# Kernel tuning notes

Hardware: AMD Instinct MI355X
Metric: run time of the kernel (lower is better)

## Reference

```python
import jax, jax.numpy as jnp
import numpy as np

B, N, K = 4, 100000, 128
Q_MIN = 0.5
S_B = 1.0
POT_SCALE = 1.0
REP_SCALE = 1.0
BETA_SCALE = 1.0
E_WEIGHT = 1.0
POS_WEIGHT = 1.0
TIME_WEIGHT = 1.0
HUBER_D = 2.0


def setup_inputs() -> dict:
    key = jax.random.key(0)
    ks = jax.random.split(key, 9)
    return {
        "beta": jax.random.uniform(ks[0], (B, N), dtype=jnp.float32),
        "ccoords": jax.random.normal(ks[1], (B, N, 2), dtype=jnp.float32),
        "pred_energy": jax.random.uniform(ks[2], (B, N), dtype=jnp.float32),
        "pred_pos": jax.random.normal(ks[3], (B, N, 2), dtype=jnp.float32),
        "pred_time": jax.random.uniform(ks[4], (B, N), dtype=jnp.float32),
        "t_energy": jax.random.uniform(ks[5], (B, N), dtype=jnp.float32),
        "t_pos": jax.random.normal(ks[6], (B, N, 2), dtype=jnp.float32),
        "t_time": jax.random.uniform(ks[7], (B, N), dtype=jnp.float32),
        "t_idx": jax.random.randint(ks[8], (B, N), 0, K + 1, dtype=jnp.int32),
    }


def _huber(x, d):
    a = jnp.abs(x)
    return jnp.where(a <= d, 0.5 * x * x, d * (a - 0.5 * d))


def _oc_loss(beta, ccoords, pred_energy, pred_pos, pred_time,
             t_energy, t_pos, t_time, t_idx):
    eps = 1e-4
    beta = jnp.clip(beta, eps, 1.0 - eps)
    q = jnp.arctanh(beta) ** 2 + Q_MIN                     # [B,N]

    obj = t_idx - 1                                        # -1 = noise, 0..K-1 = object id
    M = obj[:, :, None] == jnp.arange(K, dtype=jnp.int32)  # [B,N,K] bool membership
    Mf = M.astype(q.dtype)
    obj_exists = jnp.any(M, axis=1)                        # [B,K]
    exf = obj_exists.astype(q.dtype)

    # condensation point per object = member hit with max charge q (segment argmax)
    q_masked = jnp.where(M, q[:, :, None], -1.0)           # [B,N,K]
    alpha = jnp.argmax(q_masked, axis=1)                   # [B,K]
    x_alpha = jnp.take_along_axis(ccoords, alpha[:, :, None], axis=1)  # [B,K,2]
    q_alpha = jnp.take_along_axis(q, alpha, axis=1)        # [B,K]
    beta_alpha = jnp.take_along_axis(beta, alpha, axis=1)  # [B,K]

    # pairwise hit <-> condensation-point distances, [B,N,K]
    diff = ccoords[:, :, None, :] - x_alpha[:, None, :, :]
    dist = jnp.sqrt(jnp.sum(diff * diff, axis=-1) + 1e-12)

    qq = q[:, :, None] * q_alpha[:, None, :] * exf[:, None, :]
    v_att = qq * (dist * dist) * Mf
    v_rep = qq * jax.nn.relu(1.0 - dist) * (1.0 - Mf)
    n_tot = jnp.asarray(B * N, q.dtype)
    L_att = jnp.sum(v_att) / n_tot
    L_rep = jnp.sum(v_rep) / n_tot

    # beta loss: pull condensation-point betas to 1, suppress noise betas
    n_obj = jnp.maximum(jnp.sum(exf), 1.0)
    L_beta_obj = jnp.sum((1.0 - beta_alpha) * exf) / n_obj
    noise = (t_idx == 0).astype(q.dtype)
    L_noise = jnp.sum(beta * noise) / jnp.maximum(jnp.sum(noise), 1.0)
    L_beta = L_beta_obj + S_B * L_noise

    # payload losses, beta-weighted over non-noise hits
    p = (jnp.arctanh(beta) ** 2) * (1.0 - noise)           # [B,N]
    p_sum = jnp.maximum(jnp.sum(p), 1e-6)
    L_energy = jnp.sum(p * _huber(pred_energy - t_energy, HUBER_D)) / p_sum
    L_pos = jnp.sum(p * jnp.sum((pred_pos - t_pos) ** 2, axis=-1)) / p_sum
    L_time = jnp.sum(p * (pred_time - t_time) ** 2) / p_sum

    return (POT_SCALE * L_att + REP_SCALE * L_rep + BETA_SCALE * L_beta
            + E_WEIGHT * L_energy + POS_WEIGHT * L_pos + TIME_WEIGHT * L_time)


def reference(beta, ccoords, pred_energy, pred_pos, pred_time,
              t_energy, t_pos, t_time, t_idx):
    return _oc_loss(beta, ccoords, pred_energy, pred_pos, pred_time,
                    t_energy, t_pos, t_time, t_idx)
```

## Files before the change

kernel.cpp:

```cpp
#include <hip/hip_runtime.h>
#include <math.h>

#define BB 4
#define NN 100000
#define KK 128
#define HB 512
#define HH 4
#define GX 49
#define NBLK (GX * BB)
#define PB 64


typedef float v2f __attribute__((ext_vector_type(2)));

#if __has_builtin(__builtin_elementwise_fma)
#define FMA2(a, b, c) __builtin_elementwise_fma((a), (b), (c))
#else
static __device__ __forceinline__ v2f fma2_(v2f a, v2f b, v2f c) {
    v2f r; r.x = __builtin_fmaf(a.x, b.x, c.x); r.y = __builtin_fmaf(a.y, b.y, c.y);
    return r;
}
#define FMA2 fma2_
#endif

#if __has_builtin(__builtin_elementwise_max)
#define MAX2(a, b) __builtin_elementwise_max((a), (b))
#else
static __device__ __forceinline__ v2f max2_(v2f a, v2f b) {
    v2f r; r.x = fmaxf(a.x, b.x); r.y = fmaxf(a.y, b.y);
    return r;
}
#define MAX2 max2_
#endif

__device__ __forceinline__ float clipb(float b) {
    return fminf(fmaxf(b, 1e-4f), 1.0f - 1e-4f);
}

__device__ __forceinline__ unsigned long long mkkey(float bf, unsigned n) {
    unsigned hi = __float_as_uint(clipb(bf));
    return ((unsigned long long)hi << 32) |
           (unsigned long long)(0xFFFFFFFFu - n);
}

__global__ void __launch_bounds__(256) k_argmax(
    const float4* __restrict__ beta4, const int4* __restrict__ tidx4,
    unsigned long long* __restrict__ pk_part, unsigned int* __restrict__ cnt) {
    int b = blockIdx.y;
    __shared__ unsigned long long smax[KK];
    for (int t = threadIdx.x; t < KK; t += 256) smax[t] = 0ULL;
    if (blockIdx.x == 0 && b == 0 && threadIdx.x == 0) *cnt = 0u;
    __syncthreads();
    const float4* b4 = beta4 + (size_t)b * (NN / 4);
    const int4*   t4 = tidx4 + (size_t)b * (NN / 4);
    for (int i = blockIdx.x * 256 + threadIdx.x; i < NN / 4; i += PB * 256) {
        float4 bv = b4[i];
        int4   tv = t4[i];
        unsigned n0 = 4u * (unsigned)i;
        if (tv.x > 0) atomicMax(&smax[tv.x - 1], mkkey(bv.x, n0));
        if (tv.y > 0) atomicMax(&smax[tv.y - 1], mkkey(bv.y, n0 + 1));
        if (tv.z > 0) atomicMax(&smax[tv.z - 1], mkkey(bv.z, n0 + 2));
        if (tv.w > 0) atomicMax(&smax[tv.w - 1], mkkey(bv.w, n0 + 3));
    }
    __syncthreads();
    if (threadIdx.x < KK)
        pk_part[((size_t)b * PB + blockIdx.x) * KK + threadIdx.x] =
            smax[threadIdx.x];
}

__global__ void __launch_bounds__(HB) k_main(
    const float*  __restrict__ beta, const float2* __restrict__ cc,
    const float*  __restrict__ pe,   const float2* __restrict__ pp,
    const float*  __restrict__ pt,   const float*  __restrict__ te,
    const float2* __restrict__ tp,   const float*  __restrict__ tt,
    const int*    __restrict__ tidx,
    const unsigned long long* __restrict__ pk_part,
    unsigned long long* __restrict__ final_packed,
    float* __restrict__ part, unsigned int* __restrict__ cnt,
    float* __restrict__ out) {
    int b = blockIdx.y;
    __shared__ v2f sox[KK / 2];
    __shared__ v2f soy[KK / 2];
    __shared__ v2f soq[KK / 2];
    __shared__ float sred[8][8];
    __shared__ unsigned s_last;
    float* sax = (float*)sox;
    float* say = (float*)soy;
    float* saq = (float*)soq;

    if (threadIdx.x < KK) {
        const unsigned long long* src =
            pk_part + ((size_t)b * PB) * KK + threadIdx.x;
        unsigned long long v = 0ULL;
        #pragma unroll 8
        for (int pb = 0; pb < PB; ++pb) {
            unsigned long long u = src[(size_t)pb * KK];
            v = (u > v) ? u : v;
        }
        if (blockIdx.x == 0) final_packed[b * KK + threadIdx.x] = v;
        float x = 0.f, y = 0.f, qz = 0.f;
        if (v) {
            unsigned n = 0xFFFFFFFFu - (unsigned)(v & 0xFFFFFFFFu);
            float ba = __uint_as_float((unsigned)(v >> 32));
            float at = atanhf(ba);
            float2 c = cc[b * NN + (int)n];
            x = c.x; y = c.y; qz = at * at + 0.5f;
        }
        sax[threadIdx.x] = x;
        say[threadIdx.x] = y;
        saq[threadIdx.x] = qz;
    }

    int base = blockIdx.x * (HB * HH) + threadIdx.x;
    bool vv[HH]; int ii[HH]; float rp[HH];
    v2f cx2[HH], cy2[HH];
    #pragma unroll
    for (int h = 0; h < HH; ++h) {
        int n = base + h * HB;
        vv[h] = n < NN;
        ii[h] = b * NN + (vv[h] ? n : 0);
        float2 c = cc[ii[h]];
        cx2[h].x = c.x; cx2[h].y = c.x;
        cy2[h].x = c.y; cy2[h].y = c.y;
        rp[h] = 0.f;
    }
    __syncthreads();

    const v2f eps2 = {1e-12f, 1e-12f};
    const v2f one2 = {1.0f, 1.0f};
    const v2f zero2 = {0.0f, 0.0f};

    #pragma unroll 2
    for (int k2 = 0; k2 < KK / 2; ++k2) {
        v2f ox = sox[k2], oy = soy[k2], oq = soq[k2];
        #pragma unroll
        for (int h = 0; h < HH; ++h) {
            v2f dx = cx2[h] - ox;
            v2f dy = cy2[h] - oy;
            v2f s  = FMA2(dx, dx, FMA2(dy, dy, eps2));
            v2f d;
            d.x = __builtin_amdgcn_sqrtf(s.x);
            d.y = __builtin_amdgcn_sqrtf(s.y);
            v2f r = MAX2(one2 - d, zero2);
            rp[h] = fmaf(oq.x, r.x, rp[h]);
            rp[h] = fmaf(oq.y, r.y, rp[h]);
        }
    }

    float p_att = 0.f, p_rep = 0.f, p_nb = 0.f, p_nc = 0.f;
    float p_ps = 0.f, p_e = 0.f, p_pos = 0.f, p_tm = 0.f;

    #pragma unroll
    for (int h = 0; h < HH; ++h) {
        if (!vv[h]) continue;
        int   idx = ii[h];
        float rep = rp[h];
        float bc  = clipb(beta[idx]);
        float at  = atanhf(bc);
        float at2 = at * at;
        float q   = at2 + 0.5f;
        int   ti  = tidx[idx];
        int   obj = ti - 1;

        if (obj >= 0) {
            float ox = sax[obj], oy = say[obj], oqz = saq[obj];
            float dx = cx2[h].x - ox, dy = cy2[h].x - oy;
            float s = fmaf(dx, dx, fmaf(dy, dy, 1e-12f));
            float d = __builtin_amdgcn_sqrtf(s);
            rep   -= oqz * fmaxf(1.0f - d, 0.0f);
            p_att += q * (oqz * s);
        }
        p_rep += q * rep;

        if (ti == 0) {
            p_nb += bc;
            p_nc += 1.0f;
        } else {
            p_ps += at2;
            float de = pe[idx] - te[idx];
            float a  = fabsf(de);
            float hb = (a <= 2.0f) ? (0.5f * de * de) : (2.0f * (a - 1.0f));
            p_e  += at2 * hb;
            float2 ppv = pp[idx], tpv = tp[idx];
            float dpx = ppv.x - tpv.x, dpy = ppv.y - tpv.y;
            p_pos += at2 * (dpx * dpx + dpy * dpy);
            float dt = pt[idx] - tt[idx];
            p_tm += at2 * dt * dt;
        }
    }

    float vals[8] = {p_att, p_rep, p_nb, p_nc, p_ps, p_e, p_pos, p_tm};
    int lane = threadIdx.x & 63, wave = threadIdx.x >> 6;
    #pragma unroll
    for (int i = 0; i < 8; ++i) {
        float v = vals[i];
        #pragma unroll
        for (int off = 32; off > 0; off >>= 1) v += __shfl_down(v, off, 64);
        if (lane == 0) sred[wave][i] = v;
    }
    __syncthreads();
    if (threadIdx.x < 8) {
        float s = 0.f;
        #pragma unroll
        for (int w = 0; w < HB / 64; ++w) s += sred[w][threadIdx.x];
        part[(b * GX + blockIdx.x) * 8 + threadIdx.x] = s;
    }
    __syncthreads();

    if (threadIdx.x == 0) {
        __threadfence();
        unsigned prev = atomicAdd(cnt, 1u);
        s_last = (prev == (unsigned)(NBLK - 1)) ? 1u : 0u;
    }
    __syncthreads();
    if (s_last) {
        __threadfence();
        if (threadIdx.x < 64) {
            int flane = threadIdx.x;

            float nobj = 0.f, sba = 0.f;
            for (int t = flane; t < BB * KK; t += 64) {
                unsigned long long v = final_packed[t];
                if (v) {
                    nobj += 1.f;
                    sba  += 1.0f - __uint_as_float((unsigned)(v >> 32));
                }
            }
            #pragma unroll
            for (int off = 32; off > 0; off >>= 1) {
                nobj += __shfl_xor(nobj, off, 64);
                sba  += __shfl_xor(sba, off, 64);
            }

            int comp = flane & 7;
            float v = 0.f;
            for (int r = flane >> 3; r < NBLK; r += 8)
                v += part[r * 8 + comp];
            v += __shfl_xor(v, 8, 64);
            v += __shfl_xor(v, 16, 64);
            v += __shfl_xor(v, 32, 64);
            float tot[8];
            #pragma unroll
            for (int c = 0; c < 8; ++c) tot[c] = __shfl(v, c, 64);

            if (flane == 0) {
                float inv_n  = 1.0f / (float)(BB * NN);
                float L_beta = sba / fmaxf(nobj, 1.0f) +
                               tot[2] / fmaxf(tot[3], 1.0f);
                float p_sum  = fmaxf(tot[4], 1e-6f);
                out[0] = tot[0] * inv_n + tot[1] * inv_n + L_beta +
                         (tot[5] + tot[6] + tot[7]) / p_sum;
            }
        }
    }
}

extern "C" void kernel_launch(void* const* d_in, const int* in_sizes, int n_in,
                              void* d_out, int out_size, void* d_ws, size_t ws_size,
                              hipStream_t stream) {
    const float*  beta = (const float*)d_in[0];
    const float2* cc   = (const float2*)d_in[1];
    const float*  pe   = (const float*)d_in[2];
    const float2* pp   = (const float2*)d_in[3];
    const float*  pt   = (const float*)d_in[4];
    const float*  te   = (const float*)d_in[5];
    const float2* tp   = (const float2*)d_in[6];
    const float*  tt   = (const float*)d_in[7];
    const int*    ti   = (const int*)d_in[8];

    unsigned long long* pk_part      = (unsigned long long*)d_ws;
    unsigned long long* final_packed = (unsigned long long*)((char*)d_ws + 262144);
    float*              part         = (float*)((char*)d_ws + 266240);
    unsigned int*       cnt          = (unsigned int*)((char*)d_ws + 272512);
    float*              out          = (float*)d_out;

    k_argmax<<<dim3(PB, BB), 256, 0, stream>>>(
        (const float4*)beta, (const int4*)ti, pk_part, cnt);
    k_main<<<dim3(GX, BB), HB, 0, stream>>>(
        beta, cc, pe, pp, pt, te, tp, tt, ti,
        pk_part, final_packed, part, cnt, out);
}
```

Baseline: 115.1 us.

## Fuse argmax and main pass into one cooperative kernel with grid sync

Merges the segment-argmax kernel into the main kernel. Each block now computes per-object maxima over its own hits, writes per-block partials, and meets the other blocks at a grid-wide barrier before reducing them. Beta, t_idx and coordinates are read once and kept in registers for both phases, and the payload inputs are prefetched before the distance loop. This removes one kernel launch and a second pass over beta/t_idx, at the cost of a cooperative-launch grid sync and higher register pressure.

```diff
diff --git a/kernel.cpp b/kernel.cpp
--- a/kernel.cpp
+++ b/kernel.cpp
@@ -1,5 +1,8 @@
 #include <hip/hip_runtime.h>
+#include <hip/hip_cooperative_groups.h>
 #include <math.h>
+
+namespace cg = cooperative_groups;
 
 #define BB 4
 #define NN 100000
@@ -8,7 +11,6 @@
 #define HH 4
 #define GX 49
 #define NBLK (GX * BB)
-#define PB 64
 
 
 typedef float v2f __attribute__((ext_vector_type(2)));
@@ -43,42 +45,18 @@
            (unsigned long long)(0xFFFFFFFFu - n);
 }
 
-__global__ void __launch_bounds__(256) k_argmax(
-    const float4* __restrict__ beta4, const int4* __restrict__ tidx4,
-    unsigned long long* __restrict__ pk_part, unsigned int* __restrict__ cnt) {
-    int b = blockIdx.y;
-    __shared__ unsigned long long smax[KK];
-    for (int t = threadIdx.x; t < KK; t += 256) smax[t] = 0ULL;
-    if (blockIdx.x == 0 && b == 0 && threadIdx.x == 0) *cnt = 0u;
-    __syncthreads();
-    const float4* b4 = beta4 + (size_t)b * (NN / 4);
-    const int4*   t4 = tidx4 + (size_t)b * (NN / 4);
-    for (int i = blockIdx.x * 256 + threadIdx.x; i < NN / 4; i += PB * 256) {
-        float4 bv = b4[i];
-        int4   tv = t4[i];
-        unsigned n0 = 4u * (unsigned)i;
-        if (tv.x > 0) atomicMax(&smax[tv.x - 1], mkkey(bv.x, n0));
-        if (tv.y > 0) atomicMax(&smax[tv.y - 1], mkkey(bv.y, n0 + 1));
-        if (tv.z > 0) atomicMax(&smax[tv.z - 1], mkkey(bv.z, n0 + 2));
-        if (tv.w > 0) atomicMax(&smax[tv.w - 1], mkkey(bv.w, n0 + 3));
-    }
-    __syncthreads();
-    if (threadIdx.x < KK)
-        pk_part[((size_t)b * PB + blockIdx.x) * KK + threadIdx.x] =
-            smax[threadIdx.x];
-}
-
-__global__ void __launch_bounds__(HB) k_main(
+__global__ void __launch_bounds__(HB) k_fused(
     const float*  __restrict__ beta, const float2* __restrict__ cc,
     const float*  __restrict__ pe,   const float2* __restrict__ pp,
     const float*  __restrict__ pt,   const float*  __restrict__ te,
     const float2* __restrict__ tp,   const float*  __restrict__ tt,
     const int*    __restrict__ tidx,
-    const unsigned long long* __restrict__ pk_part,
+    unsigned long long* __restrict__ pk_part,
     unsigned long long* __restrict__ final_packed,
     float* __restrict__ part, unsigned int* __restrict__ cnt,
     float* __restrict__ out) {
     int b = blockIdx.y;
+    __shared__ unsigned long long smax[KK];
     __shared__ v2f sox[KK / 2];
     __shared__ v2f soy[KK / 2];
     __shared__ v2f soq[KK / 2];
@@ -88,12 +66,42 @@
     float* say = (float*)soy;
     float* saq = (float*)soq;
 
+    int base = blockIdx.x * (HB * HH) + threadIdx.x;
+    bool vv[HH]; int ii[HH]; float rp[HH];
+    float bt[HH]; int tiv[HH];
+    v2f cx2[HH], cy2[HH];
+    #pragma unroll
+    for (int h = 0; h < HH; ++h) {
+        int n = base + h * HB;
+        vv[h] = n < NN;
+        ii[h] = b * NN + (vv[h] ? n : 0);
+        float2 c = cc[ii[h]];
+        cx2[h].x = c.x; cx2[h].y = c.x;
+        cy2[h].x = c.y; cy2[h].y = c.y;
+        bt[h]  = beta[ii[h]];
+        tiv[h] = tidx[ii[h]];
+        rp[h] = 0.f;
+    }
+    if (threadIdx.x < KK) smax[threadIdx.x] = 0ULL;
+    if (blockIdx.x == 0 && b == 0 && threadIdx.x == 0) atomicExch(cnt, 0u);
+    __syncthreads();
+    #pragma unroll
+    for (int h = 0; h < HH; ++h)
+        if (vv[h] && tiv[h] > 0)
+            atomicMax(&smax[tiv[h] - 1], mkkey(bt[h], (unsigned)(base + h * HB)));
+    __syncthreads();
+    if (threadIdx.x < KK)
+        pk_part[((size_t)b * GX + blockIdx.x) * KK + threadIdx.x] =
+            smax[threadIdx.x];
+    __threadfence();
+    cg::this_grid().sync();
+
     if (threadIdx.x < KK) {
         const unsigned long long* src =
-            pk_part + ((size_t)b * PB) * KK + threadIdx.x;
+            pk_part + ((size_t)b * GX) * KK + threadIdx.x;
         unsigned long long v = 0ULL;
-        #pragma unroll 8
-        for (int pb = 0; pb < PB; ++pb) {
+        #pragma unroll 7
+        for (int pb = 0; pb < GX; ++pb) {
             unsigned long long u = src[(size_t)pb * KK];
             v = (u > v) ? u : v;
         }
@@ -111,18 +119,13 @@
         saq[threadIdx.x] = qz;
     }
 
-    int base = blockIdx.x * (HB * HH) + threadIdx.x;
-    bool vv[HH]; int ii[HH]; float rp[HH];
-    v2f cx2[HH], cy2[HH];
+    float pe_[HH], te_[HH], pt_[HH], tt_[HH];
+    float2 pp_[HH], tp_[HH];
     #pragma unroll
     for (int h = 0; h < HH; ++h) {
-        int n = base + h * HB;
-        vv[h] = n < NN;
-        ii[h] = b * NN + (vv[h] ? n : 0);
-        float2 c = cc[ii[h]];
-        cx2[h].x = c.x; cx2[h].y = c.x;
-        cy2[h].x = c.y; cy2[h].y = c.y;
-        rp[h] = 0.f;
+        pe_[h] = pe[ii[h]]; te_[h] = te[ii[h]];
+        pt_[h] = pt[ii[h]]; tt_[h] = tt[ii[h]];
+        pp_[h] = pp[ii[h]]; tp_[h] = tp[ii[h]];
     }
     __syncthreads();
 
@@ -153,13 +156,12 @@
     #pragma unroll
     for (int h = 0; h < HH; ++h) {
         if (!vv[h]) continue;
-        int   idx = ii[h];
         float rep = rp[h];
-        float bc  = clipb(beta[idx]);
+        float bc  = clipb(bt[h]);
         float at  = atanhf(bc);
         float at2 = at * at;
         float q   = at2 + 0.5f;
-        int   ti  = tidx[idx];
+        int   ti  = tiv[h];
         int   obj = ti - 1;
 
         if (obj >= 0) {
@@ -177,14 +179,13 @@
             p_nc += 1.0f;
         } else {
             p_ps += at2;
-            float de = pe[idx] - te[idx];
+            float de = pe_[h] - te_[h];
             float a  = fabsf(de);
             float hb = (a <= 2.0f) ? (0.5f * de * de) : (2.0f * (a - 1.0f));
             p_e  += at2 * hb;
-            float2 ppv = pp[idx], tpv = tp[idx];
-            float dpx = ppv.x - tpv.x, dpy = ppv.y - tpv.y;
+            float dpx = pp_[h].x - tp_[h].x, dpy = pp_[h].y - tp_[h].y;
             p_pos += at2 * (dpx * dpx + dpy * dpy);
-            float dt = pt[idx] - tt[idx];
+            float dt = pt_[h] - tt_[h];
             p_tm += at2 * dt * dt;
         }
     }
@@ -269,14 +270,17 @@
     const int*    ti   = (const int*)d_in[8];
 
     unsigned long long* pk_part      = (unsigned long long*)d_ws;
-    unsigned long long* final_packed = (unsigned long long*)((char*)d_ws + 262144);
-    float*              part         = (float*)((char*)d_ws + 266240);
-    unsigned int*       cnt          = (unsigned int*)((char*)d_ws + 272512);
+    unsigned long long* final_packed = (unsigned long long*)((char*)d_ws + 200704);
+    float*              part         = (float*)((char*)d_ws + 204800);
+    unsigned int*       cnt          = (unsigned int*)((char*)d_ws + 211072);
     float*              out          = (float*)d_out;
 
-    k_argmax<<<dim3(PB, BB), 256, 0, stream>>>(
-        (const float4*)beta, (const int4*)ti, pk_part, cnt);
-    k_main<<<dim3(GX, BB), HB, 0, stream>>>(
-        beta, cc, pe, pp, pt, te, tp, tt, ti,
-        pk_part, final_packed, part, cnt, out);
-}
+    void* args[] = {
+        (void*)&beta, (void*)&cc, (void*)&pe, (void*)&pp, (void*)&pt,
+        (void*)&te, (void*)&tp, (void*)&tt, (void*)&ti,
+        (void*)&pk_part, (void*)&final_packed, (void*)&part,
+        (void*)&cnt, (void*)&out,
+    };
+    hipLaunchCooperativeKernel((const void*)k_fused, dim3(GX, BB), dim3(HB),
+                               args, 0, stream);
+}
```

Result: slower. 169.2 us (+47.1%).
